# Kernel optimization log

Measured on AMD Instinct MI355X. Metric: run time of the kernel, lower is better.

## Reference

```python
import jax, jax.numpy as jnp
import numpy as np

N_NODES = 20000
N_EDGES = 320000
C = 64  # classes
NEG_SLOPE = 0.2  # DGL GATConv default


def setup_inputs() -> dict:
    key = jax.random.key(0)
    ks = jax.random.split(key, 32)
    dims = [C, 2 * C, 4 * C, 8 * C, 16 * C]
    inp = {}
    inp["feat"] = jax.random.normal(ks[0], (N_NODES, C), jnp.float32)
    k = 1
    for i in range(4):
        din, dout = dims[i], dims[i + 1]
        scale = 1.0 / np.sqrt(din)
        inp[f"W{i+1}"] = jax.random.normal(ks[k], (din, dout), jnp.float32) * scale; k += 1
        inp[f"al{i+1}"] = jax.random.normal(ks[k], (dout,), jnp.float32) * 0.1; k += 1
        inp[f"ar{i+1}"] = jax.random.normal(ks[k], (dout,), jnp.float32) * 0.1; k += 1
        inp[f"b{i+1}"] = jnp.zeros((dout,), jnp.float32)
    inp["relW"] = jax.random.normal(ks[k], (16 * C, C), jnp.float32) * (1.0 / np.sqrt(16 * C)); k += 1
    inp["relB"] = jnp.zeros((C,), jnp.float32)
    inp["src"] = jax.random.randint(ks[k], (N_EDGES,), 0, N_NODES, jnp.int32); k += 1
    inp["dst"] = jax.random.randint(ks[k], (N_EDGES,), 0, N_NODES, jnp.int32); k += 1
    inp["rel"] = jnp.ones((C,), jnp.int32)
    inp["order"] = 1023
    return inp


def _gat_layer(x, W, al, ar, b, src, dst, n_nodes):
    """DGL GATConv (num_heads=1, allow_zero_in_degree=True, activation=tanh)."""
    h = x @ W                                   # [N, D] projected features
    el = h @ al                                 # [N] attn_l score per node
    er = h @ ar                                 # [N] attn_r score per node
    e = jax.nn.leaky_relu(el[src] + er[dst], NEG_SLOPE)          # [E]
    # segment (edge) softmax over incoming edges of each dst node
    m = jax.ops.segment_max(e, dst, num_segments=n_nodes)        # [N]
    ex = jnp.exp(e - m[dst])                                      # [E]
    s = jax.ops.segment_sum(ex, dst, num_segments=n_nodes)       # [N]
    alpha = ex / s[dst]                                           # [E]
    # gather neighbor messages, weight by attention, scatter-add to dst
    out = jax.ops.segment_sum(h[src] * alpha[:, None], dst, num_segments=n_nodes)  # [N, D]
    return jnp.tanh(out + b)


def reference(feat, W1, al1, ar1, b1, W2, al2, ar2, b2, W3, al3, ar3, b3,
              W4, al4, ar4, b4, relW, relB, src, dst, rel, order):
    n = feat.shape[0]
    h = _gat_layer(feat, W1, al1, ar1, b1, src, dst, n)
    h = _gat_layer(h, W2, al2, ar2, b2, src, dst, n)
    h = _gat_layer(h, W3, al3, ar3, b3, src, dst, n)
    h = _gat_layer(h, W4, al4, ar4, b4, src, dst, n)
    embeddings = h[: order + 1]                  # first order+1 node embeddings
    pooling = jnp.mean(embeddings, axis=0)       # [16C]
    logits = pooling @ relW + relB               # [C]
    nz = jnp.nonzero(rel, size=rel.shape[0])[0]  # static-size nonzero (rel is all-ones)
    return logits[nz]
```

## Files before the change

kernel.cpp:

```cpp
#include <hip/hip_runtime.h>
#include <hip/hip_bf16.h>

#define NN 20000
#define NE 320000
#define MPAD 20096
#define ORD 1024
#define NB 79

typedef __hip_bfloat16 bf16;
typedef __attribute__((ext_vector_type(8))) short bf16x8;
typedef __attribute__((ext_vector_type(4))) float f32x4;

#define SCOPE_AGENT __HIP_MEMORY_SCOPE_AGENT

static __device__ __forceinline__ float b2f(bf16 x) { return __bfloat162float(x); }
static __device__ __forceinline__ float bfbits2f(short s) {
    unsigned int u = ((unsigned int)(unsigned short)s) << 16;
    float f; __builtin_memcpy(&f, &u, 4); return f;
}
static __device__ __forceinline__ short f2bfbits(float v) {
    bf16 h = __float2bfloat16(v);
    short s; __builtin_memcpy(&s, &h, 2); return s;
}
static __device__ __forceinline__ unsigned short f2bfu(float v) {
    bf16 h = __float2bfloat16(v);
    unsigned short s; __builtin_memcpy(&s, &h, 2); return s;
}
static __device__ __forceinline__ int aload(const int* p) {
    return __hip_atomic_load(p, __ATOMIC_RELAXED, SCOPE_AGENT);
}
static __device__ __forceinline__ void astore(int* p, int v) {
    __hip_atomic_store(p, v, __ATOMIC_RELAXED, SCOPE_AGENT);
}
static __device__ __forceinline__ void aadd(int* p, int v) {
    __hip_atomic_fetch_add(p, v, __ATOMIC_RELAXED, SCOPE_AGENT);
}
static __device__ __forceinline__ float aloadf(const float* p) {
    return __hip_atomic_load(p, __ATOMIC_RELAXED, SCOPE_AGENT);
}

__global__ void setup_all(const float* __restrict__ feat,
                          const float* __restrict__ W1, const float* __restrict__ al1, const float* __restrict__ ar1,
                          const float* __restrict__ W2, const float* __restrict__ al2, const float* __restrict__ ar2,
                          const float* __restrict__ W3, const float* __restrict__ al3, const float* __restrict__ ar3,
                          const float* __restrict__ W4, const float* __restrict__ al4, const float* __restrict__ ar4,
                          bf16* __restrict__ featb, bf16* __restrict__ wt1,
                          bf16* __restrict__ wt2, bf16* __restrict__ wt3,
                          bf16* __restrict__ wt4, int* __restrict__ counts,
                          int* __restrict__ hglob, int* __restrict__ syncbuf,
                          float* __restrict__ walbuf, float* __restrict__ warbuf) {
    int b = blockIdx.x;
    if (b < 960) {
        const float *W, *al, *ar; int dout, k; float *wal, *war;
        if (b < 64)       { W = W1; al = al1; ar = ar1; dout = 128;  k = b;       wal = walbuf;        war = warbuf; }
        else if (b < 192) { W = W2; al = al2; ar = ar2; dout = 256;  k = b - 64;  wal = walbuf + 512;  war = warbuf + 512; }
        else if (b < 448) { W = W3; al = al3; ar = ar3; dout = 512;  k = b - 192; wal = walbuf + 1024; war = warbuf + 1024; }
        else              { W = W4; al = al4; ar = ar4; dout = 1024; k = b - 448; wal = walbuf + 1536; war = warbuf + 1536; }
        const float* row = W + (long)k * dout;
        float sl = 0.f, sr = 0.f;
        for (int j = threadIdx.x; j < dout; j += 256) {
            float w = row[j];
            sl += w * al[j];
            sr += w * ar[j];
        }
        __shared__ float sbl[256], sbr[256];
        sbl[threadIdx.x] = sl; sbr[threadIdx.x] = sr;
        __syncthreads();
        for (int st = 128; st > 0; st >>= 1) {
            if (threadIdx.x < st) {
                sbl[threadIdx.x] += sbl[threadIdx.x + st];
                sbr[threadIdx.x] += sbr[threadIdx.x + st];
            }
            __syncthreads();
        }
        if (threadIdx.x == 0) { wal[k] = sbl[0]; war[k] = sbr[0]; }
        return;
    }
    int i = (b - 960) * 256 + threadIdx.x;
    if (i < NN) counts[i] = 0;
    if (i < 256) { hglob[i] = 0; syncbuf[i] = 0; }
    if (i < 1280000) { featb[i] = __float2bfloat16(feat[i]); return; }
    i -= 1280000;
    if (i < 8192)  { int r = i >> 7,  c = i & 127;  wt1[c * 64 + r]  = __float2bfloat16(W1[i]); return; }
    i -= 8192;
    if (i < 32768) { int r = i >> 8,  c = i & 255;  wt2[c * 128 + r] = __float2bfloat16(W2[i]); return; }
    i -= 32768;
    if (i < 131072){ int r = i >> 9,  c = i & 511;  wt3[c * 256 + r] = __float2bfloat16(W3[i]); return; }
    i -= 131072;
    if (i < 524288){ int r = i >> 10, c = i & 1023; wt4[c * 512 + r] = __float2bfloat16(W4[i]); return; }
}

__global__ void csr_build(const int* __restrict__ dst, int* __restrict__ counts,
                          int* __restrict__ blocksums, int* __restrict__ blockbase,
                          int* __restrict__ hglob,
                          int* __restrict__ offsets, int* __restrict__ cursor,
                          int* __restrict__ curg, int* __restrict__ sync) {
    int b = blockIdx.x, tid = threadIdx.x;
    if (b < 1250) {
        int i = b * 256 + tid;
        atomicAdd(&counts[dst[i]], 1);
        __syncthreads();
        if (tid == 0) aadd(&sync[(b & 7) * 16], 1);
        return;
    }
    if (b == 1250 + NB) {
        if (tid == 0) while (aload(&sync[128]) != NB) __builtin_amdgcn_s_sleep(2);
        __syncthreads();
        __shared__ int hs[256], bs[256];
        int orig = aload(&hglob[tid]);
        hs[tid] = orig;
        __syncthreads();
        for (int st = 1; st < 256; st <<= 1) {
            int u = (tid >= st) ? hs[tid - st] : 0;
            __syncthreads();
            hs[tid] += u;
            __syncthreads();
        }
        curg[tid] = hs[tid] - orig;
        int v = (tid < NB) ? aload(&blocksums[tid]) : 0;
        bs[tid] = v;
        __syncthreads();
        for (int st = 1; st < 256; st <<= 1) {
            int u = (tid >= st) ? bs[tid - st] : 0;
            __syncthreads();
            bs[tid] += u;
            __syncthreads();
        }
        if (tid < NB) astore(&blockbase[tid], bs[tid] - v);
        __syncthreads();
        if (tid == 0) astore(&sync[132], 1);
        return;
    }
    int pb = b - 1250;
    if (tid == 0) {
        for (;;) {
            int t = 0;
            #pragma unroll
            for (int k = 0; k < 8; k++) t += aload(&sync[k * 16]);
            if (t == 1250) break;
            __builtin_amdgcn_s_sleep(2);
        }
    }
    __syncthreads();
    __shared__ int sc[256], hh[256];
    hh[tid] = 0;
    int i = pb * 256 + tid;
    int c = (i < NN) ? aload(&counts[i]) : 0;
    sc[tid] = c;
    __syncthreads();
    for (int st = 1; st < 256; st <<= 1) {
        int u = (tid >= st) ? sc[tid - st] : 0;
        __syncthreads();
        sc[tid] += u;
        __syncthreads();
    }
    if (tid == 255) astore(&blocksums[pb], sc[255]);
    if (i < NN) { int d = c > 255 ? 255 : c; atomicAdd(&hh[d], 1); }
    __syncthreads();
    if (hh[tid] > 0) atomicAdd(&hglob[tid], hh[tid]);
    __syncthreads();
    if (tid == 0) {
        aadd(&sync[128], 1);
        while (aload(&sync[132]) == 0) __builtin_amdgcn_s_sleep(2);
    }
    __syncthreads();
    int base = aload(&blockbase[pb]);
    int excl = base + sc[tid] - c;
    if (i < NN) { offsets[i] = excl; cursor[i] = excl; }
    if (i == NN - 1) offsets[NN] = excl + c;
}

__global__ void scatter_elr(const int* __restrict__ src, const int* __restrict__ dst,
                            int* __restrict__ cursor, int* __restrict__ esrc,
                            const int* __restrict__ counts, int* __restrict__ curg,
                            int* __restrict__ nodeperm,
                            const bf16* __restrict__ X, const float* __restrict__ wal,
                            const float* __restrict__ war, float* __restrict__ el,
                            float* __restrict__ er) {
    int b = blockIdx.x;
    if (b < 1250) {
        int i = b * 256 + threadIdx.x;
        int p = atomicAdd(&cursor[dst[i]], 1);
        esrc[p] = src[i];
        return;
    }
    if (b < 1250 + NB) {
        __shared__ int hh[256];
        __shared__ int basep[256];
        int tid = threadIdx.x;
        hh[tid] = 0;
        __syncthreads();
        int i = (b - 1250) * 256 + tid;
        int d = 0, rank = 0;
        bool valid = (i < NN);
        if (valid) {
            d = counts[i]; if (d > 255) d = 255;
            rank = atomicAdd(&hh[d], 1);
        }
        __syncthreads();
        if (hh[tid] > 0) basep[tid] = atomicAdd(&curg[tid], hh[tid]);
        __syncthreads();
        if (valid) nodeperm[basep[d] + rank] = i;
        return;
    }
    int idx = (b - 1250 - NB) * 256 + threadIdx.x;
    int node = idx >> 6;
    int lane = threadIdx.x & 63;
    if (node >= NN) return;
    float x = bfbits2f(*((const short*)X + (long)node * 64 + lane));
    float sl = x * wal[lane];
    float sr = x * war[lane];
    #pragma unroll
    for (int o = 32; o > 0; o >>= 1) {
        sl += __shfl_down(sl, o);
        sr += __shfl_down(sr, o);
    }
    if (lane == 0) { el[node] = sl; er[node] = sr; }
}

__global__ void aggregate_sm(const bf16* __restrict__ X,
                             const float* __restrict__ el, const float* __restrict__ er,
                             const int* __restrict__ esrc, const int* __restrict__ off,
                             const int* __restrict__ perm, float* __restrict__ zbuf, int zn,
                             bf16* __restrict__ Y, int din, int log2chunks, int nmax) {
    __shared__ __attribute__((aligned(16))) float alds[32][68];
    {
        int z = blockIdx.x * 256 + threadIdx.x;
        if (z < zn) zbuf[z] = 0.f;
    }
    int chunk = blockIdx.x & ((1 << log2chunks) - 1);
    int nb = blockIdx.x >> log2chunks;
    int sub = threadIdx.x >> 3, sl = threadIdx.x & 7;
    int slot = nb * 32 + sub;
    if (slot >= nmax) return;
    int node = perm ? perm[slot] : slot;
    int s = off[node], e = off[node + 1];
    int deg = e - s;
    bool fast = (deg <= 64);

    float erd = (deg > 0) ? er[node] : 0.f;
    float vmax = -1e30f, inv = 0.f;
    if (fast) {
        float v[8];
        #pragma unroll
        for (int t = 0; t < 8; t++) {
            v[t] = -1e30f;
            int idx = sl + 8 * t;
            if (idx < deg) {
                float x = el[esrc[s + idx]] + erd;
                v[t] = x >= 0.f ? x : 0.2f * x;
            }
            vmax = fmaxf(vmax, v[t]);
        }
        #pragma unroll
        for (int o = 1; o < 8; o <<= 1) vmax = fmaxf(vmax, __shfl_xor(vmax, o));
        float ssum = 0.f;
        #pragma unroll
        for (int t = 0; t < 8; t++) {
            int idx = sl + 8 * t;
            if (idx < deg) { v[t] = __expf(v[t] - vmax); ssum += v[t]; }
        }
        #pragma unroll
        for (int o = 1; o < 8; o <<= 1) ssum += __shfl_xor(ssum, o);
        inv = 1.f / ssum;
        #pragma unroll
        for (int t = 0; t < 8; t++) {
            int idx = sl + 8 * t;
            if (idx < deg) alds[sub][idx] = v[t] * inv;
        }
    } else {
        for (int j = s + sl; j < e; j += 8) {
            float x = el[esrc[j]] + erd;
            x = x >= 0.f ? x : 0.2f * x;
            vmax = fmaxf(vmax, x);
        }
        #pragma unroll
        for (int o = 1; o < 8; o <<= 1) vmax = fmaxf(vmax, __shfl_xor(vmax, o));
        float ssum = 0.f;
        for (int j = s + sl; j < e; j += 8) {
            float x = el[esrc[j]] + erd;
            x = x >= 0.f ? x : 0.2f * x;
            ssum += __expf(x - vmax);
        }
        #pragma unroll
        for (int o = 1; o < 8; o <<= 1) ssum += __shfl_xor(ssum, o);
        inv = 1.f / ssum;
    }

    const short* xb = (const short*)X + chunk * 64 + sl * 8;
    float acc[8] = {0.f,0.f,0.f,0.f,0.f,0.f,0.f,0.f};
    int j = s;
    if (fast) {
        for (; j + 8 <= e; j += 8) {
            int ofs = j - s;
            f32x4 a0 = *(const f32x4*)&alds[sub][ofs];
            f32x4 a1 = *(const f32x4*)&alds[sub][ofs + 4];
            int r[8]; bf16x8 w[8];
            #pragma unroll
            for (int q = 0; q < 8; q++) r[q] = esrc[j + q];
            #pragma unroll
            for (int q = 0; q < 8; q++) w[q] = *(const bf16x8*)(xb + (long)r[q] * din);
            #pragma unroll
            for (int q = 0; q < 4; q++)
                #pragma unroll
                for (int v = 0; v < 8; v++) acc[v] += a0[q] * bfbits2f(w[q][v]);
            #pragma unroll
            for (int q = 0; q < 4; q++)
                #pragma unroll
                for (int v = 0; v < 8; v++) acc[v] += a1[q] * bfbits2f(w[4 + q][v]);
        }
        for (; j + 4 <= e; j += 4) {
            int ofs = j - s;
            f32x4 a0 = *(const f32x4*)&alds[sub][ofs];
            int r[4]; bf16x8 w[4];
            #pragma unroll
            for (int q = 0; q < 4; q++) r[q] = esrc[j + q];
            #pragma unroll
            for (int q = 0; q < 4; q++) w[q] = *(const bf16x8*)(xb + (long)r[q] * din);
            #pragma unroll
            for (int q = 0; q < 4; q++)
                #pragma unroll
                for (int v = 0; v < 8; v++) acc[v] += a0[q] * bfbits2f(w[q][v]);
        }
        for (; j < e; j++) {
            float a = alds[sub][j - s];
            bf16x8 w = *(const bf16x8*)(xb + (long)esrc[j] * din);
            #pragma unroll
            for (int v = 0; v < 8; v++) acc[v] += a * bfbits2f(w[v]);
        }
    } else {
        for (; j + 8 <= e; j += 8) {
            int r[8]; float a[8]; bf16x8 w[8];
            #pragma unroll
            for (int q = 0; q < 8; q++) r[q] = esrc[j + q];
            #pragma unroll
            for (int q = 0; q < 8; q++) {
                float x = el[r[q]] + erd;
                x = x >= 0.f ? x : 0.2f * x;
                a[q] = __expf(x - vmax) * inv;
            }
            #pragma unroll
            for (int q = 0; q < 8; q++) w[q] = *(const bf16x8*)(xb + (long)r[q] * din);
            #pragma unroll
            for (int q = 0; q < 8; q++)
                #pragma unroll
                for (int v = 0; v < 8; v++) acc[v] += a[q] * bfbits2f(w[q][v]);
        }
        for (; j < e; j++) {
            int r = esrc[j];
            float x = el[r] + erd;
            x = x >= 0.f ? x : 0.2f * x;
            float a = __expf(x - vmax) * inv;
            bf16x8 w = *(const bf16x8*)(xb + (long)r * din);
            #pragma unroll
            for (int v = 0; v < 8; v++) acc[v] += a * bfbits2f(w[v]);
        }
    }
    short outv[8];
    #pragma unroll
    for (int v = 0; v < 8; v++) outv[v] = f2bfbits(acc[v]);
    bf16x8 store;
    __builtin_memcpy(&store, outv, sizeof(store));
    *(bf16x8*)((short*)Y + (long)node * din + chunk * 64 + sl * 8) = store;
}

__global__ __launch_bounds__(256, 4)
void gemm_k64(const bf16* __restrict__ A, const bf16* __restrict__ WT,
              const float* __restrict__ bias, bf16* __restrict__ C,
              const float* __restrict__ wal, const float* __restrict__ war,
              float* __restrict__ elp, float* __restrict__ erp) {
    int gw = blockIdx.x * 4 + (threadIdx.x >> 6);
    if (gw >= 2500) return;
    int r0 = (gw >> 1) << 4;
    int col0 = (gw & 1) << 6;
    int lane = threadIdx.x & 63;
    int m = lane & 15, quad = lane >> 4;

    const short* Ab = (const short*)A + (long)(r0 + m) * 64 + quad * 8;
    bf16x8 a0 = *(const bf16x8*)(Ab);
    bf16x8 a1 = *(const bf16x8*)(Ab + 32);

    f32x4 acc[4];
    bf16x8 b0[4], b1[4];
    #pragma unroll
    for (int t = 0; t < 4; t++) {
        acc[t] = (f32x4){0.f, 0.f, 0.f, 0.f};
        const short* Bb = (const short*)WT + (long)(col0 + t * 16 + m) * 64 + quad * 8;
        b0[t] = *(const bf16x8*)(Bb);
        b1[t] = *(const bf16x8*)(Bb + 32);
    }
    #pragma unroll
    for (int t = 0; t < 4; t++) {
        acc[t] = __builtin_amdgcn_mfma_f32_16x16x32_bf16(a0, b0[t], acc[t], 0, 0, 0);
        acc[t] = __builtin_amdgcn_mfma_f32_16x16x32_bf16(a1, b1[t], acc[t], 0, 0, 0);
    }

    float sl4[4] = {0.f, 0.f, 0.f, 0.f};
    float sr4[4] = {0.f, 0.f, 0.f, 0.f};
    #pragma unroll
    for (int t = 0; t < 4; t++) {
        int col = col0 + t * 16 + m;
        float bb = bias[col];
        float wl = wal[col], wrr = war[col];
        #pragma unroll
        for (int r = 0; r < 4; r++) {
            float v = tanhf(acc[t][r] + bb);
            sl4[r] += v * wl;
            sr4[r] += v * wrr;
            float vn = __shfl_xor(v, 1);
            if ((m & 1) == 0) {
                unsigned int pk = (unsigned int)f2bfu(v) | ((unsigned int)f2bfu(vn) << 16);
                int row = r0 + quad * 4 + r;
                *(unsigned int*)((short*)C + (long)row * 128 + col) = pk;
            }
        }
    }
    #pragma unroll
    for (int r = 0; r < 4; r++) {
        float s1 = sl4[r], s2 = sr4[r];
        #pragma unroll
        for (int o = 1; o < 16; o <<= 1) {
            s1 += __shfl_xor(s1, o);
            s2 += __shfl_xor(s2, o);
        }
        if (m == 0) {
            int row = r0 + quad * 4 + r;
            atomicAdd(&elp[row], s1);
            atomicAdd(&erp[row], s2);
        }
    }
}

__global__ __launch_bounds__(256, 4)
void gemm_tiled(const bf16* __restrict__ A, const bf16* __restrict__ WT,
                const float* __restrict__ bias, bf16* __restrict__ C,
                const float* __restrict__ wal, const float* __restrict__ war,
                float* __restrict__ elp, float* __restrict__ erp,
                float* __restrict__ poolacc,
                const float* __restrict__ relW, const float* __restrict__ relB,
                const int* __restrict__ order, const int* __restrict__ rel,
                float* __restrict__ headout,
                int M, int K, int N, int ncols, int nrows) {
    __shared__ short smem[16384];
    short* As = smem;
    short* Bs = smem + 8192;
    int g = blockIdx.x;
    int rowTile = ((g >> 3) / ncols) * 8 + (g & 7);
    int colTile = (g >> 3) % ncols;
    if (rowTile >= nrows) return;
    int row0 = rowTile << 7, col0 = colTile << 7;
    int tid = threadIdx.x;
    int lane = tid & 63, wave = tid >> 6;
    int wr = (wave >> 1) << 6;
    int wc = (wave & 1) << 6;
    int m = lane & 15, quad = lane >> 4;

    f32x4 acc[4][4];
    #pragma unroll
    for (int i = 0; i < 4; i++)
        #pragma unroll
        for (int j = 0; j < 4; j++) acc[i][j] = (f32x4){0.f, 0.f, 0.f, 0.f};

    const short* Ab = (const short*)A;
    const short* Bb = (const short*)WT;
    long ga[4], gb[4];
    #pragma unroll
    for (int n = 0; n < 4; n++) {
        int chunk = n * 256 + tid;
        int row = chunk >> 3;
        int qg = (chunk & 7) ^ (row & 7);
        ga[n] = (long)(row0 + row) * K + qg * 8;
        gb[n] = (long)(col0 + row) * K + qg * 8;
    }

    typedef const __attribute__((address_space(1))) void cgvoid;
    typedef __attribute__((address_space(3))) void lvoid;

    for (int k0 = 0; k0 < K; k0 += 64) {
        __syncthreads();
        #pragma unroll
        for (int n = 0; n < 4; n++)
            __builtin_amdgcn_global_load_lds((cgvoid*)(Ab + ga[n] + k0),
                                             (lvoid*)(As + (n * 256 + tid) * 8), 16, 0, 0);
        #pragma unroll
        for (int n = 0; n < 4; n++)
            __builtin_amdgcn_global_load_lds((cgvoid*)(Bb + gb[n] + k0),
                                             (lvoid*)(Bs + (n * 256 + tid) * 8), 16, 0, 0);
        __syncthreads();
        #pragma unroll
        for (int h = 0; h < 2; h++) {
            bf16x8 af[4], bfr[4];
            #pragma unroll
            for (int s = 0; s < 4; s++) {
                int ra = wr + s * 16 + m;
                int sa = (h * 4 + quad) ^ (ra & 7);
                af[s] = *(const bf16x8*)(As + ra * 64 + sa * 8);
                int rb = wc + s * 16 + m;
                int sb = (h * 4 + quad) ^ (rb & 7);
                bfr[s] = *(const bf16x8*)(Bs + rb * 64 + sb * 8);
            }
            #pragma unroll
            for (int i = 0; i < 4; i++)
                #pragma unroll
                for (int j = 0; j < 4; j++)
                    acc[i][j] = __builtin_amdgcn_mfma_f32_16x16x32_bf16(af[i], bfr[j], acc[i][j], 0, 0, 0);
        }
    }

    float bb[4], walr[4], warr[4];
    #pragma unroll
    for (int j = 0; j < 4; j++) {
        int col = col0 + wc + j * 16 + m;
        bb[j] = bias[col];
        if (elp) { walr[j] = wal[col]; warr[j] = war[col]; }
    }
    float colsum[4] = {0.f, 0.f, 0.f, 0.f};
    __syncthreads();
    short* myep = smem + wave * 1152;
    #pragma unroll
    for (int i = 0; i < 4; i++) {
        float sl4[4] = {0.f, 0.f, 0.f, 0.f};
        float sr4[4] = {0.f, 0.f, 0.f, 0.f};
        #pragma unroll
        for (int j = 0; j < 4; j++) {
            #pragma unroll
            for (int r = 0; r < 4; r++) {
                float v = tanhf(acc[i][j][r] + bb[j]);
                if (elp) { sl4[r] += v * walr[j]; sr4[r] += v * warr[j]; }
                if (poolacc) colsum[j] += v;
                float vn = __shfl_xor(v, 1);
                if ((m & 1) == 0) {
                    unsigned int pk = (unsigned int)f2bfu(v) | ((unsigned int)f2bfu(vn) << 16);
                    *(unsigned int*)(myep + (quad * 4 + r) * 72 + j * 16 + m) = pk;
                }
            }
        }
        #pragma unroll
        for (int pass = 0; pass < 2; pass++) {
            int lr = pass * 8 + (lane >> 3);
            int lc = (lane & 7) * 8;
            bf16x8 v = *(const bf16x8*)(myep + lr * 72 + lc);
            int row = row0 + wr + i * 16 + lr;
            if (row < M)
                *(bf16x8*)((short*)C + (long)row * N + col0 + wc + lc) = v;
        }
        if (elp) {
            #pragma unroll
            for (int r = 0; r < 4; r++) {
                float s1 = sl4[r], s2 = sr4[r];
                #pragma unroll
                for (int o = 1; o < 16; o <<= 1) {
                    s1 += __shfl_xor(s1, o);
                    s2 += __shfl_xor(s2, o);
                }
                if (m == 0) {
                    int row = row0 + wr + i * 16 + quad * 4 + r;
                    if (row < M) {
                        atomicAdd(&elp[row], s1);
                        atomicAdd(&erp[row], s2);
                    }
                }
            }
        }
    }
    if (poolacc) {
        #pragma unroll
        for (int j = 0; j < 4; j++) {
            float cs = colsum[j];
            cs += __shfl_xor(cs, 16);
            cs += __shfl_xor(cs, 32);
            if (quad == 0)
                atomicAdd(&poolacc[col0 + wc + j * 16 + m], cs);
        }
    }
    if (headout) {
        __syncthreads();
        __shared__ int lastf;
        if (tid == 0) {
            unsigned int old = __hip_atomic_fetch_add((unsigned int*)&poolacc[1024], 1u,
                                                      __ATOMIC_RELAXED, SCOPE_AGENT);
            lastf = (old == 63u) ? 1 : 0;
        }
        __syncthreads();
        if (!lastf) return;
        float* ps = (float*)smem;
        float (*part)[64] = (float(*)[64])(smem + 2048);
        for (int i = tid; i < 1024; i += 256) ps[i] = aloadf(&poolacc[i]);
        __syncthreads();
        int t = tid & 63, p = tid >> 6;
        const float* wp = relW + (long)p * 256 * 64 + t;
        float s = 0.f;
        #pragma unroll 8
        for (int c = 0; c < 256; c++) s += ps[p * 256 + c] * wp[(long)c * 64];
        part[p][t] = s;
        __syncthreads();
        if (tid < 64) {
            float rows = (float)(order[0] + 1);
            float lv = (part[0][tid] + part[1][tid] + part[2][tid] + part[3][tid]) / rows + relB[tid];
            int rv = rel[tid];
            unsigned long long mask = __ballot(rv != 0);
            int pos = __popcll(mask & ((1ULL << tid) - 1));
            int count = __popcll(mask);
            float l0 = __shfl(lv, 0);
            if (rv) headout[pos] = lv;
            if (tid >= count) headout[tid] = l0;
        }
    }
}

extern "C" void kernel_launch(void* const* d_in, const int* in_sizes, int n_in,
                              void* d_out, int out_size, void* d_ws, size_t ws_size,
                              hipStream_t stream) {
    const float* feat = (const float*)d_in[0];
    const float* W[4]  = {(const float*)d_in[1], (const float*)d_in[5], (const float*)d_in[9],  (const float*)d_in[13]};
    const float* al[4] = {(const float*)d_in[2], (const float*)d_in[6], (const float*)d_in[10], (const float*)d_in[14]};
    const float* ar[4] = {(const float*)d_in[3], (const float*)d_in[7], (const float*)d_in[11], (const float*)d_in[15]};
    const float* bias[4] = {(const float*)d_in[4], (const float*)d_in[8], (const float*)d_in[12], (const float*)d_in[16]};
    const float* relW = (const float*)d_in[17];
    const float* relB = (const float*)d_in[18];
    const int* src = (const int*)d_in[19];
    const int* dst = (const int*)d_in[20];
    const int* rel = (const int*)d_in[21];
    const int* order = (const int*)d_in[22];

    const int dims[5] = {64, 128, 256, 512, 1024};

    char* p = (char*)d_ws;
    auto carve = [&](size_t bytes) {
        void* r = (void*)p;
        p += (bytes + 255) & ~(size_t)255;
        return r;
    };
    bf16* xbuf = (bf16*)carve((size_t)MPAD * 1024 * sizeof(bf16));
    bf16* ybuf = (bf16*)carve((size_t)MPAD * 512 * sizeof(bf16));
    bf16* featb = (bf16*)carve((size_t)MPAD * 64 * sizeof(bf16));
    bf16* wt[4];
    for (int l = 0; l < 4; l++)
        wt[l] = (bf16*)carve((size_t)dims[l] * dims[l + 1] * sizeof(bf16));
    float* walbuf = (float*)carve(4 * 512 * sizeof(float));
    float* warbuf = (float*)carve(4 * 512 * sizeof(float));
    float* elbuf[2];
    elbuf[0] = (float*)carve((size_t)2 * NN * sizeof(float));
    elbuf[1] = (float*)carve((size_t)2 * NN * sizeof(float));
    int* counts  = (int*)carve((size_t)NN * sizeof(int));
    int* offsets = (int*)carve((size_t)(NN + 1) * sizeof(int));
    int* cursor  = (int*)carve((size_t)NN * sizeof(int));
    int* esrc    = (int*)carve((size_t)NE * sizeof(int));
    int* nodeperm = (int*)carve((size_t)NN * sizeof(int));
    int* blocksums = (int*)carve(128 * sizeof(int));
    int* blockbase = (int*)carve(128 * sizeof(int));
    int* hglob   = (int*)carve(256 * sizeof(int));
    int* curg    = (int*)carve(256 * sizeof(int));
    int* syncbuf = (int*)carve(256 * sizeof(int));
    float* poolsum = (float*)carve(1056 * sizeof(float));

    setup_all<<<960 + 7720, 256, 0, stream>>>(
        feat, W[0], al[0], ar[0], W[1], al[1], ar[1],
        W[2], al[2], ar[2], W[3], al[3], ar[3],
        featb, wt[0], wt[1], wt[2], wt[3], counts, hglob, syncbuf, walbuf, warbuf);

    csr_build<<<1250 + NB + 1, 256, 0, stream>>>(dst, counts, blocksums, blockbase,
                                                 hglob, offsets, cursor, curg, syncbuf);

    scatter_elr<<<1250 + NB + 5000, 256, 0, stream>>>(src, dst, cursor, esrc,
                                                      counts, curg, nodeperm,
                                                      featb, walbuf, warbuf,
                                                      elbuf[0], elbuf[0] + NN);

    const bf16* x = featb;
    const int nrows = MPAD / 128;
    const int nrowsPad = 160;
    const int log2c[4] = {0, 1, 2, 3};
    for (int l = 0; l < 4; l++) {
        int K = dims[l], N = dims[l + 1];
        float* elr_rd = elbuf[l & 1];
        float* elr_wr = elbuf[(l + 1) & 1];
        int nmax  = (l < 3) ? NN : ORD;
        int nodeBlocks = (nmax + 31) / 32;
        const int* aggPerm = (l < 3) ? nodeperm : nullptr;
        float* zbuf = (l < 3) ? elr_wr : poolsum;
        int zn = (l < 3) ? 2 * NN : 1025;
        aggregate_sm<<<nodeBlocks << log2c[l], 256, 0, stream>>>(
            x, elr_rd, elr_rd + NN, esrc, offsets, aggPerm, zbuf, zn, ybuf, K, log2c[l], nmax);
        int ncols = N >> 7;
        if (l == 0) {
            gemm_k64<<<625, 256, 0, stream>>>(ybuf, wt[0], bias[0], xbuf,
                                              walbuf + 512, warbuf + 512,
                                              elr_wr, elr_wr + NN);
        } else if (l < 3) {
            gemm_tiled<<<nrowsPad * ncols, 256, 0, stream>>>(
                ybuf, wt[l], bias[l], xbuf,
                walbuf + (l + 1) * 512, warbuf + (l + 1) * 512,
                elr_wr, elr_wr + NN, nullptr,
                nullptr, nullptr, nullptr, nullptr, nullptr,
                NN, K, N, ncols, nrows);
        } else {
            gemm_tiled<<<8 * ncols, 256, 0, stream>>>(
                ybuf, wt[l], bias[l], xbuf,
                nullptr, nullptr, nullptr, nullptr, poolsum,
                relW, relB, order, rel, (float*)d_out,
                ORD, K, N, ncols, 8);
        }
        x = xbuf;
    }
}
```

Before: 295.9 us.

## Fuse aggregation and GEMM per 128-row tile for first three GAT layers

Adds a fused_layer kernel that performs edge-softmax aggregation for a 128-node tile straight into LDS, then runs the MFMA GEMM with tanh, bias and el/er projection from that tile, for layers 1-3. This drops the intermediate aggregated-feature buffer round trip through global memory and one launch per layer, and writes el/er directly instead of with atomics. The degree-sorted node permutation and its histogram machinery are removed. In exchange only 157 blocks run (about 80 KB LDS each, two per CU), so the gather phase gets far less parallelism than the earlier per-chunk aggregate launches and load balance across high-degree nodes may suffer.

```diff
diff --git a/kernel.cpp b/kernel.cpp
--- a/kernel.cpp
+++ b/kernel.cpp
@@ -47,7 +47,7 @@
                           bf16* __restrict__ featb, bf16* __restrict__ wt1,
                           bf16* __restrict__ wt2, bf16* __restrict__ wt3,
                           bf16* __restrict__ wt4, int* __restrict__ counts,
-                          int* __restrict__ hglob, int* __restrict__ syncbuf,
+                          int* __restrict__ syncbuf,
                           float* __restrict__ walbuf, float* __restrict__ warbuf) {
     int b = blockIdx.x;
     if (b < 960) {
@@ -78,7 +78,7 @@
     }
     int i = (b - 960) * 256 + threadIdx.x;
     if (i < NN) counts[i] = 0;
-    if (i < 256) { hglob[i] = 0; syncbuf[i] = 0; }
+    if (i < 256) syncbuf[i] = 0;
     if (i < 1280000) { featb[i] = __float2bfloat16(feat[i]); return; }
     i -= 1280000;
     if (i < 8192)  { int r = i >> 7,  c = i & 127;  wt1[c * 64 + r]  = __float2bfloat16(W1[i]); return; }
@@ -92,9 +92,8 @@
 
 __global__ void csr_build(const int* __restrict__ dst, int* __restrict__ counts,
                           int* __restrict__ blocksums, int* __restrict__ blockbase,
-                          int* __restrict__ hglob,
                           int* __restrict__ offsets, int* __restrict__ cursor,
-                          int* __restrict__ curg, int* __restrict__ sync) {
+                          int* __restrict__ sync) {
     int b = blockIdx.x, tid = threadIdx.x;
     if (b < 1250) {
         int i = b * 256 + tid;
@@ -106,17 +105,7 @@
     if (b == 1250 + NB) {
         if (tid == 0) while (aload(&sync[128]) != NB) __builtin_amdgcn_s_sleep(2);
         __syncthreads();
-        __shared__ int hs[256], bs[256];
-        int orig = aload(&hglob[tid]);
-        hs[tid] = orig;
-        __syncthreads();
-        for (int st = 1; st < 256; st <<= 1) {
-            int u = (tid >= st) ? hs[tid - st] : 0;
-            __syncthreads();
-            hs[tid] += u;
-            __syncthreads();
-        }
-        curg[tid] = hs[tid] - orig;
+        __shared__ int bs[256];
         int v = (tid < NB) ? aload(&blocksums[tid]) : 0;
         bs[tid] = v;
         __syncthreads();
@@ -142,8 +131,7 @@
         }
     }
     __syncthreads();
-    __shared__ int sc[256], hh[256];
-    hh[tid] = 0;
+    __shared__ int sc[256];
     int i = pb * 256 + tid;
     int c = (i < NN) ? aload(&counts[i]) : 0;
     sc[tid] = c;
@@ -155,9 +143,6 @@
         __syncthreads();
     }
     if (tid == 255) astore(&blocksums[pb], sc[255]);
-    if (i < NN) { int d = c > 255 ? 255 : c; atomicAdd(&hh[d], 1); }
-    __syncthreads();
-    if (hh[tid] > 0) atomicAdd(&hglob[tid], hh[tid]);
     __syncthreads();
     if (tid == 0) {
         aadd(&sync[128], 1);
@@ -172,8 +157,6 @@
 
 __global__ void scatter_elr(const int* __restrict__ src, const int* __restrict__ dst,
                             int* __restrict__ cursor, int* __restrict__ esrc,
-                            const int* __restrict__ counts, int* __restrict__ curg,
-                            int* __restrict__ nodeperm,
                             const bf16* __restrict__ X, const float* __restrict__ wal,
                             const float* __restrict__ war, float* __restrict__ el,
                             float* __restrict__ er) {
@@ -184,26 +167,7 @@
         esrc[p] = src[i];
         return;
     }
-    if (b < 1250 + NB) {
-        __shared__ int hh[256];
-        __shared__ int basep[256];
-        int tid = threadIdx.x;
-        hh[tid] = 0;
-        __syncthreads();
-        int i = (b - 1250) * 256 + tid;
-        int d = 0, rank = 0;
-        bool valid = (i < NN);
-        if (valid) {
-            d = counts[i]; if (d > 255) d = 255;
-            rank = atomicAdd(&hh[d], 1);
-        }
-        __syncthreads();
-        if (hh[tid] > 0) basep[tid] = atomicAdd(&curg[tid], hh[tid]);
-        __syncthreads();
-        if (valid) nodeperm[basep[d] + rank] = i;
-        return;
-    }
-    int idx = (b - 1250 - NB) * 256 + threadIdx.x;
+    int idx = (b - 1250) * 256 + threadIdx.x;
     int node = idx >> 6;
     int lane = threadIdx.x & 63;
     if (node >= NN) return;
@@ -218,10 +182,283 @@
     if (lane == 0) { el[node] = sl; er[node] = sr; }
 }
 
+__global__ __launch_bounds__(256, 2)
+void fused_layer(const bf16* __restrict__ X,
+                 const float* __restrict__ el, const float* __restrict__ er,
+                 const int* __restrict__ esrc, const int* __restrict__ off,
+                 const bf16* __restrict__ WT, const float* __restrict__ bias,
+                 bf16* __restrict__ C,
+                 const float* __restrict__ wal, const float* __restrict__ war,
+                 float* __restrict__ elo, float* __restrict__ ero,
+                 int K, int ncols) {
+    __shared__ __attribute__((aligned(16))) short smem[40960];
+    short* As = smem;
+    short* Bs = smem + 32768;
+    float (*alds)[68] = (float(*)[68])Bs;
+
+    int row0 = blockIdx.x << 7;
+    int tid = threadIdx.x, lane = tid & 63, wave = tid >> 6;
+    int sub = tid >> 3, sl = tid & 7;
+    int nch = K >> 6;
+
+    for (int nb = 0; nb < 4; nb++) {
+        int nl = nb * 32 + sub;
+        int node = row0 + nl;
+        bool valid = node < NN;
+        int s = 0, deg = 0;
+        float erd = 0.f, vmax = -1e30f, inv = 0.f;
+        bool fast = true;
+        if (valid) {
+            s = off[node];
+            deg = off[node + 1] - s;
+            fast = (deg <= 64);
+            erd = (deg > 0) ? er[node] : 0.f;
+        }
+        int e = s + deg;
+        if (valid) {
+            if (fast) {
+                float v[8];
+                #pragma unroll
+                for (int t = 0; t < 8; t++) {
+                    v[t] = -1e30f;
+                    int idx = sl + 8 * t;
+                    if (idx < deg) {
+                        float x = el[esrc[s + idx]] + erd;
+                        v[t] = x >= 0.f ? x : 0.2f * x;
+                    }
+                    vmax = fmaxf(vmax, v[t]);
+                }
+                #pragma unroll
+                for (int o = 1; o < 8; o <<= 1) vmax = fmaxf(vmax, __shfl_xor(vmax, o));
+                float ssum = 0.f;
+                #pragma unroll
+                for (int t = 0; t < 8; t++) {
+                    int idx = sl + 8 * t;
+                    if (idx < deg) { v[t] = __expf(v[t] - vmax); ssum += v[t]; }
+                }
+                #pragma unroll
+                for (int o = 1; o < 8; o <<= 1) ssum += __shfl_xor(ssum, o);
+                inv = 1.f / ssum;
+                #pragma unroll
+                for (int t = 0; t < 8; t++) {
+                    int idx = sl + 8 * t;
+                    if (idx < deg) alds[sub][idx] = v[t] * inv;
+                }
+            } else {
+                for (int j = s + sl; j < e; j += 8) {
+                    float x = el[esrc[j]] + erd;
+                    x = x >= 0.f ? x : 0.2f * x;
+                    vmax = fmaxf(vmax, x);
+                }
+                #pragma unroll
+                for (int o = 1; o < 8; o <<= 1) vmax = fmaxf(vmax, __shfl_xor(vmax, o));
+                float ssum = 0.f;
+                for (int j = s + sl; j < e; j += 8) {
+                    float x = el[esrc[j]] + erd;
+                    x = x >= 0.f ? x : 0.2f * x;
+                    ssum += __expf(x - vmax);
+                }
+                #pragma unroll
+                for (int o = 1; o < 8; o <<= 1) ssum += __shfl_xor(ssum, o);
+                inv = 1.f / ssum;
+            }
+        }
+        for (int c = 0; c < nch; c++) {
+            float acc[8] = {0.f,0.f,0.f,0.f,0.f,0.f,0.f,0.f};
+            if (valid && deg > 0) {
+                const short* xb = (const short*)X + c * 64 + sl * 8;
+                int j = s;
+                if (fast) {
+                    for (; j + 8 <= e; j += 8) {
+                        int ofs = j - s;
+                        f32x4 a0 = *(const f32x4*)&alds[sub][ofs];
+                        f32x4 a1 = *(const f32x4*)&alds[sub][ofs + 4];
+                        int r[8]; bf16x8 w[8];
+                        #pragma unroll
+                        for (int q = 0; q < 8; q++) r[q] = esrc[j + q];
+                        #pragma unroll
+                        for (int q = 0; q < 8; q++) w[q] = *(const bf16x8*)(xb + (long)r[q] * K);
+                        #pragma unroll
+                        for (int q = 0; q < 4; q++)
+                            #pragma unroll
+                            for (int v = 0; v < 8; v++) acc[v] += a0[q] * bfbits2f(w[q][v]);
+                        #pragma unroll
+                        for (int q = 0; q < 4; q++)
+                            #pragma unroll
+                            for (int v = 0; v < 8; v++) acc[v] += a1[q] * bfbits2f(w[4 + q][v]);
+                    }
+                    for (; j + 4 <= e; j += 4) {
+                        int ofs = j - s;
+                        f32x4 a0 = *(const f32x4*)&alds[sub][ofs];
+                        int r[4]; bf16x8 w[4];
+                        #pragma unroll
+                        for (int q = 0; q < 4; q++) r[q] = esrc[j + q];
+                        #pragma unroll
+                        for (int q = 0; q < 4; q++) w[q] = *(const bf16x8*)(xb + (long)r[q] * K);
+                        #pragma unroll
+                        for (int q = 0; q < 4; q++)
+                            #pragma unroll
+                            for (int v = 0; v < 8; v++) acc[v] += a0[q] * bfbits2f(w[q][v]);
+                    }
+                    for (; j < e; j++) {
+                        float a = alds[sub][j - s];
+                        bf16x8 w = *(const bf16x8*)(xb + (long)esrc[j] * K);
+                        #pragma unroll
+                        for (int v = 0; v < 8; v++) acc[v] += a * bfbits2f(w[v]);
+                    }
+                } else {
+                    for (; j < e; j++) {
+                        int r = esrc[j];
+                        float x = el[r] + erd;
+                        x = x >= 0.f ? x : 0.2f * x;
+                        float a = __expf(x - vmax) * inv;
+                        bf16x8 w = *(const bf16x8*)(xb + (long)r * K);
+                        #pragma unroll
+                        for (int v = 0; v < 8; v++) acc[v] += a * bfbits2f(w[v]);
+                    }
+                }
+            }
+            short outv[8];
+            #pragma unroll
+            for (int v = 0; v < 8; v++) outv[v] = f2bfbits(acc[v]);
+            bf16x8 st;
+            __builtin_memcpy(&st, outv, sizeof(st));
+            int qs = (c * 8 + sl) ^ (nl & 7);
+            *(bf16x8*)(As + nl * K + qs * 8) = st;
+        }
+    }
+    __syncthreads();
+
+    int m = lane & 15, quad = lane >> 4;
+    int wr = (wave >> 1) << 6;
+    int wc = (wave & 1) << 6;
+    float slacc[4][4], sracc[4][4];
+    #pragma unroll
+    for (int i = 0; i < 4; i++)
+        #pragma unroll
+        for (int r = 0; r < 4; r++) { slacc[i][r] = 0.f; sracc[i][r] = 0.f; }
+
+    typedef const __attribute__((address_space(1))) void cgvoid;
+    typedef __attribute__((address_space(3))) void lvoid;
+    int N = ncols << 7;
+
+    for (int ct = 0; ct < ncols; ct++) {
+        int col0 = ct << 7;
+        f32x4 acc[4][4];
+        #pragma unroll
+        for (int i = 0; i < 4; i++)
+            #pragma unroll
+            for (int j = 0; j < 4; j++) acc[i][j] = (f32x4){0.f, 0.f, 0.f, 0.f};
+
+        for (int k0 = 0; k0 < K; k0 += 64) {
+            __syncthreads();
+            #pragma unroll
+            for (int n = 0; n < 4; n++) {
+                int chunk = n * 256 + tid;
+                int brow = chunk >> 3;
+                int qg = (chunk & 7) ^ (brow & 7);
+                __builtin_amdgcn_global_load_lds(
+                    (cgvoid*)((const short*)WT + (long)(col0 + brow) * K + k0 + qg * 8),
+                    (lvoid*)(Bs + (n * 256 + tid) * 8), 16, 0, 0);
+            }
+            __syncthreads();
+            int kq = k0 >> 3;
+            #pragma unroll
+            for (int h = 0; h < 2; h++) {
+                bf16x8 af[4], bfr[4];
+                #pragma unroll
+                for (int ss = 0; ss < 4; ss++) {
+                    int ra = wr + ss * 16 + m;
+                    int sa = (kq + h * 4 + quad) ^ (ra & 7);
+                    af[ss] = *(const bf16x8*)(As + ra * K + sa * 8);
+                    int rb = wc + ss * 16 + m;
+                    int sb = (h * 4 + quad) ^ (rb & 7);
+                    bfr[ss] = *(const bf16x8*)(Bs + rb * 64 + sb * 8);
+                }
+                #pragma unroll
+                for (int i = 0; i < 4; i++)
+                    #pragma unroll
+                    for (int j = 0; j < 4; j++)
+                        acc[i][j] = __builtin_amdgcn_mfma_f32_16x16x32_bf16(af[i], bfr[j], acc[i][j], 0, 0, 0);
+            }
+        }
+        __syncthreads();
+
+        float bb[4], walr[4], warr[4];
+        #pragma unroll
+        for (int j = 0; j < 4; j++) {
+            int col = col0 + wc + j * 16 + m;
+            bb[j] = bias[col];
+            walr[j] = wal[col]; warr[j] = war[col];
+        }
+        short* myep = Bs + wave * 1152;
+        #pragma unroll
+        for (int i = 0; i < 4; i++) {
+            #pragma unroll
+            for (int j = 0; j < 4; j++) {
+                #pragma unroll
+                for (int r = 0; r < 4; r++) {
+                    float v = tanhf(acc[i][j][r] + bb[j]);
+                    slacc[i][r] += v * walr[j];
+                    sracc[i][r] += v * warr[j];
+                    float vn = __shfl_xor(v, 1);
+                    if ((m & 1) == 0) {
+                        unsigned int pk = (unsigned int)f2bfu(v) | ((unsigned int)f2bfu(vn) << 16);
+                        *(unsigned int*)(myep + (quad * 4 + r) * 72 + j * 16 + m) = pk;
+                    }
+                }
+            }
+            #pragma unroll
+            for (int pass = 0; pass < 2; pass++) {
+                int lr = pass * 8 + (lane >> 3);
+                int lc = (lane & 7) * 8;
+                bf16x8 v = *(const bf16x8*)(myep + lr * 72 + lc);
+                int row = row0 + wr + i * 16 + lr;
+                if (row < NN)
+                    *(bf16x8*)((short*)C + (long)row * N + col0 + wc + lc) = v;
+            }
+        }
+    }
+
+    __syncthreads();
+    float* scr = (float*)smem;
+    #pragma unroll
+    for (int i = 0; i < 4; i++) {
+        #pragma unroll
+        for (int r = 0; r < 4; r++) {
+            float s1 = slacc[i][r], s2 = sracc[i][r];
+            #pragma unroll
+            for (int o = 1; o < 16; o <<= 1) {
+                s1 += __shfl_xor(s1, o);
+                s2 += __shfl_xor(s2, o);
+            }
+            slacc[i][r] = s1; sracc[i][r] = s2;
+            if ((wave & 1) == 1 && m == 0) {
+                int lr = wr + i * 16 + quad * 4 + r;
+                scr[lr * 2] = s1; scr[lr * 2 + 1] = s2;
+            }
+        }
+    }
+    __syncthreads();
+    if ((wave & 1) == 0 && m == 0) {
+        #pragma unroll
+        for (int i = 0; i < 4; i++)
+            #pragma unroll
+            for (int r = 0; r < 4; r++) {
+                int lr = wr + i * 16 + quad * 4 + r;
+                int row = row0 + lr;
+                if (row < NN) {
+                    elo[row] = slacc[i][r] + scr[lr * 2];
+                    ero[row] = sracc[i][r] + scr[lr * 2 + 1];
+                }
+            }
+    }
+}
+
 __global__ void aggregate_sm(const bf16* __restrict__ X,
                              const float* __restrict__ el, const float* __restrict__ er,
                              const int* __restrict__ esrc, const int* __restrict__ off,
-                             const int* __restrict__ perm, float* __restrict__ zbuf, int zn,
+                             float* __restrict__ zbuf, int zn,
                              bf16* __restrict__ Y, int din, int log2chunks, int nmax) {
     __shared__ __attribute__((aligned(16))) float alds[32][68];
     {
@@ -233,7 +470,7 @@
     int sub = threadIdx.x >> 3, sl = threadIdx.x & 7;
     int slot = nb * 32 + sub;
     if (slot >= nmax) return;
-    int node = perm ? perm[slot] : slot;
+    int node = slot;
     int s = off[node], e = off[node + 1];
     int deg = e - s;
     bool fast = (deg <= 64);
@@ -329,23 +566,6 @@
             for (int v = 0; v < 8; v++) acc[v] += a * bfbits2f(w[v]);
         }
     } else {
-        for (; j + 8 <= e; j += 8) {
-            int r[8]; float a[8]; bf16x8 w[8];
-            #pragma unroll
-            for (int q = 0; q < 8; q++) r[q] = esrc[j + q];
-            #pragma unroll
-            for (int q = 0; q < 8; q++) {
-                float x = el[r[q]] + erd;
-                x = x >= 0.f ? x : 0.2f * x;
-                a[q] = __expf(x - vmax) * inv;
-            }
-            #pragma unroll
-            for (int q = 0; q < 8; q++) w[q] = *(const bf16x8*)(xb + (long)r[q] * din);
-            #pragma unroll
-            for (int q = 0; q < 8; q++)
-                #pragma unroll
-                for (int v = 0; v < 8; v++) acc[v] += a[q] * bfbits2f(w[q][v]);
-        }
         for (; j < e; j++) {
             int r = esrc[j];
             float x = el[r] + erd;
@@ -365,77 +585,8 @@
 }
 
 __global__ __launch_bounds__(256, 4)
-void gemm_k64(const bf16* __restrict__ A, const bf16* __restrict__ WT,
-              const float* __restrict__ bias, bf16* __restrict__ C,
-              const float* __restrict__ wal, const float* __restrict__ war,
-              float* __restrict__ elp, float* __restrict__ erp) {
-    int gw = blockIdx.x * 4 + (threadIdx.x >> 6);
-    if (gw >= 2500) return;
-    int r0 = (gw >> 1) << 4;
-    int col0 = (gw & 1) << 6;
-    int lane = threadIdx.x & 63;
-    int m = lane & 15, quad = lane >> 4;
-
-    const short* Ab = (const short*)A + (long)(r0 + m) * 64 + quad * 8;
-    bf16x8 a0 = *(const bf16x8*)(Ab);
-    bf16x8 a1 = *(const bf16x8*)(Ab + 32);
-
-    f32x4 acc[4];
-    bf16x8 b0[4], b1[4];
-    #pragma unroll
-    for (int t = 0; t < 4; t++) {
-        acc[t] = (f32x4){0.f, 0.f, 0.f, 0.f};
-        const short* Bb = (const short*)WT + (long)(col0 + t * 16 + m) * 64 + quad * 8;
-        b0[t] = *(const bf16x8*)(Bb);
-        b1[t] = *(const bf16x8*)(Bb + 32);
-    }
-    #pragma unroll
-    for (int t = 0; t < 4; t++) {
-        acc[t] = __builtin_amdgcn_mfma_f32_16x16x32_bf16(a0, b0[t], acc[t], 0, 0, 0);
-        acc[t] = __builtin_amdgcn_mfma_f32_16x16x32_bf16(a1, b1[t], acc[t], 0, 0, 0);
-    }
-
-    float sl4[4] = {0.f, 0.f, 0.f, 0.f};
-    float sr4[4] = {0.f, 0.f, 0.f, 0.f};
-    #pragma unroll
-    for (int t = 0; t < 4; t++) {
-        int col = col0 + t * 16 + m;
-        float bb = bias[col];
-        float wl = wal[col], wrr = war[col];
-        #pragma unroll
-        for (int r = 0; r < 4; r++) {
-            float v = tanhf(acc[t][r] + bb);
-            sl4[r] += v * wl;
-            sr4[r] += v * wrr;
-            float vn = __shfl_xor(v, 1);
-            if ((m & 1) == 0) {
-                unsigned int pk = (unsigned int)f2bfu(v) | ((unsigned int)f2bfu(vn) << 16);
-                int row = r0 + quad * 4 + r;
-                *(unsigned int*)((short*)C + (long)row * 128 + col) = pk;
-            }
-        }
-    }
-    #pragma unroll
-    for (int r = 0; r < 4; r++) {
-        float s1 = sl4[r], s2 = sr4[r];
-        #pragma unroll
-        for (int o = 1; o < 16; o <<= 1) {
-            s1 += __shfl_xor(s1, o);
-            s2 += __shfl_xor(s2, o);
-        }
-        if (m == 0) {
-            int row = r0 + quad * 4 + r;
-            atomicAdd(&elp[row], s1);
-            atomicAdd(&erp[row], s2);
-        }
-    }
-}
-
-__global__ __launch_bounds__(256, 4)
 void gemm_tiled(const bf16* __restrict__ A, const bf16* __restrict__ WT,
                 const float* __restrict__ bias, bf16* __restrict__ C,
-                const float* __restrict__ wal, const float* __restrict__ war,
-                float* __restrict__ elp, float* __restrict__ erp,
                 float* __restrict__ poolacc,
                 const float* __restrict__ relW, const float* __restrict__ relB,
                 const int* __restrict__ order, const int* __restrict__ rel,
@@ -507,27 +658,20 @@
         }
     }
 
-    float bb[4], walr[4], warr[4];
+    float bb[4];
     #pragma unroll
-    for (int j = 0; j < 4; j++) {
-        int col = col0 + wc + j * 16 + m;
-        bb[j] = bias[col];
-        if (elp) { walr[j] = wal[col]; warr[j] = war[col]; }
-    }
+    for (int j = 0; j < 4; j++) bb[j] = bias[col0 + wc + j * 16 + m];
     float colsum[4] = {0.f, 0.f, 0.f, 0.f};
     __syncthreads();
     short* myep = smem + wave * 1152;
     #pragma unroll
     for (int i = 0; i < 4; i++) {
-        float sl4[4] = {0.f, 0.f, 0.f, 0.f};
-        float sr4[4] = {0.f, 0.f, 0.f, 0.f};
         #pragma unroll
         for (int j = 0; j < 4; j++) {
             #pragma unroll
             for (int r = 0; r < 4; r++) {
                 float v = tanhf(acc[i][j][r] + bb[j]);
-                if (elp) { sl4[r] += v * walr[j]; sr4[r] += v * warr[j]; }
-                if (poolacc) colsum[j] += v;
+                colsum[j] += v;
                 float vn = __shfl_xor(v, 1);
                 if ((m & 1) == 0) {
                     unsigned int pk = (unsigned int)f2bfu(v) | ((unsigned int)f2bfu(vn) << 16);
@@ -544,67 +688,45 @@
             if (row < M)
                 *(bf16x8*)((short*)C + (long)row * N + col0 + wc + lc) = v;
         }
-        if (elp) {
-            #pragma unroll
-            for (int r = 0; r < 4; r++) {
-                float s1 = sl4[r], s2 = sr4[r];
-                #pragma unroll
-                for (int o = 1; o < 16; o <<= 1) {
-                    s1 += __shfl_xor(s1, o);
-                    s2 += __shfl_xor(s2, o);
-                }
-                if (m == 0) {
-                    int row = row0 + wr + i * 16 + quad * 4 + r;
-                    if (row < M) {
-                        atomicAdd(&elp[row], s1);
-                        atomicAdd(&erp[row], s2);
-                    }
-                }
-            }
-        }
-    }
-    if (poolacc) {
-        #pragma unroll
-        for (int j = 0; j < 4; j++) {
-            float cs = colsum[j];
-            cs += __shfl_xor(cs, 16);
-            cs += __shfl_xor(cs, 32);
-            if (quad == 0)
-                atomicAdd(&poolacc[col0 + wc + j * 16 + m], cs);
-        }
-    }
-    if (headout) {
-        __syncthreads();
-        __shared__ int lastf;
-        if (tid == 0) {
-            unsigned int old = __hip_atomic_fetch_add((unsigned int*)&poolacc[1024], 1u,
-                                                      __ATOMIC_RELAXED, SCOPE_AGENT);
-            lastf = (old == 63u) ? 1 : 0;
-        }
-        __syncthreads();
-        if (!lastf) return;
-        float* ps = (float*)smem;
-        float (*part)[64] = (float(*)[64])(smem + 2048);
-        for (int i = tid; i < 1024; i += 256) ps[i] = aloadf(&poolacc[i]);
-        __syncthreads();
-        int t = tid & 63, p = tid >> 6;
-        const float* wp = relW + (long)p * 256 * 64 + t;
-        float s = 0.f;
-        #pragma unroll 8
-        for (int c = 0; c < 256; c++) s += ps[p * 256 + c] * wp[(long)c * 64];
-        part[p][t] = s;
-        __syncthreads();
-        if (tid < 64) {
-            float rows = (float)(order[0] + 1);
-            float lv = (part[0][tid] + part[1][tid] + part[2][tid] + part[3][tid]) / rows + relB[tid];
-            int rv = rel[tid];
-            unsigned long long mask = __ballot(rv != 0);
-            int pos = __popcll(mask & ((1ULL << tid) - 1));
-            int count = __popcll(mask);
-            float l0 = __shfl(lv, 0);
-            if (rv) headout[pos] = lv;
-            if (tid >= count) headout[tid] = l0;
-        }
+    }
+    #pragma unroll
+    for (int j = 0; j < 4; j++) {
+        float cs = colsum[j];
+        cs += __shfl_xor(cs, 16);
+        cs += __shfl_xor(cs, 32);
+        if (quad == 0)
+            atomicAdd(&poolacc[col0 + wc + j * 16 + m], cs);
+    }
+    __syncthreads();
+    __shared__ int lastf;
+    if (tid == 0) {
+        unsigned int old = __hip_atomic_fetch_add((unsigned int*)&poolacc[1024], 1u,
+                                                  __ATOMIC_RELAXED, SCOPE_AGENT);
+        lastf = (old == 63u) ? 1 : 0;
+    }
+    __syncthreads();
+    if (!lastf) return;
+    float* ps = (float*)smem;
+    float (*part)[64] = (float(*)[64])(smem + 2048);
+    for (int i = tid; i < 1024; i += 256) ps[i] = aloadf(&poolacc[i]);
+    __syncthreads();
+    int t = tid & 63, p = tid >> 6;
+    const float* wp = relW + (long)p * 256 * 64 + t;
+    float s = 0.f;
+    #pragma unroll 8
+    for (int c = 0; c < 256; c++) s += ps[p * 256 + c] * wp[(long)c * 64];
+    part[p][t] = s;
+    __syncthreads();
+    if (tid < 64) {
+        float rows = (float)(order[0] + 1);
+        float lv = (part[0][tid] + part[1][tid] + part[2][tid] + part[3][tid]) / rows + relB[tid];
+        int rv = rel[tid];
+        unsigned long long mask = __ballot(rv != 0);
+        int pos = __popcll(mask & ((1ULL << tid) - 1));
+        int count = __popcll(mask);
+        float l0 = __shfl(lv, 0);
+        if (rv) headout[pos] = lv;
+        if (tid >= count) headout[tid] = l0;
     }
 }
 
@@ -631,8 +753,9 @@
         p += (bytes + 255) & ~(size_t)255;
         return r;
     };
-    bf16* xbuf = (bf16*)carve((size_t)MPAD * 1024 * sizeof(bf16));
-    bf16* ybuf = (bf16*)carve((size_t)MPAD * 512 * sizeof(bf16));
+    bf16* xA = (bf16*)carve((size_t)MPAD * 512 * sizeof(bf16));
+    bf16* xB = (bf16*)carve((size_t)MPAD * 256 * sizeof(bf16));
+    bf16* y4 = (bf16*)carve((size_t)ORD * 512 * sizeof(bf16));
     bf16* featb = (bf16*)carve((size_t)MPAD * 64 * sizeof(bf16));
     bf16* wt[4];
     for (int l = 0; l < 4; l++)
@@ -646,61 +769,40 @@
     int* offsets = (int*)carve((size_t)(NN + 1) * sizeof(int));
     int* cursor  = (int*)carve((size_t)NN * sizeof(int));
     int* esrc    = (int*)carve((size_t)NE * sizeof(int));
-    int* nodeperm = (int*)carve((size_t)NN * sizeof(int));
     int* blocksums = (int*)carve(128 * sizeof(int));
     int* blockbase = (int*)carve(128 * sizeof(int));
-    int* hglob   = (int*)carve(256 * sizeof(int));
-    int* curg    = (int*)carve(256 * sizeof(int));
     int* syncbuf = (int*)carve(256 * sizeof(int));
     float* poolsum = (float*)carve(1056 * sizeof(float));
 
     setup_all<<<960 + 7720, 256, 0, stream>>>(
         feat, W[0], al[0], ar[0], W[1], al[1], ar[1],
         W[2], al[2], ar[2], W[3], al[3], ar[3],
-        featb, wt[0], wt[1], wt[2], wt[3], counts, hglob, syncbuf, walbuf, warbuf);
+        featb, wt[0], wt[1], wt[2], wt[3], counts, syncbuf, walbuf, warbuf);
 
     csr_build<<<1250 + NB + 1, 256, 0, stream>>>(dst, counts, blocksums, blockbase,
-                                                 hglob, offsets, cursor, curg, syncbuf);
-
-    scatter_elr<<<1250 + NB + 5000, 256, 0, stream>>>(src, dst, cursor, esrc,
-                                                      counts, curg, nodeperm,
-                                                      featb, walbuf, warbuf,
-                                                      elbuf[0], elbuf[0] + NN);
-
-    const bf16* x = featb;
-    const int nrows = MPAD / 128;
-    const int nrowsPad = 160;
-    const int log2c[4] = {0, 1, 2, 3};
-    for (int l = 0; l < 4; l++) {
-        int K = dims[l], N = dims[l + 1];
-        float* elr_rd = elbuf[l & 1];
-        float* elr_wr = elbuf[(l + 1) & 1];
-        int nmax  = (l < 3) ? NN : ORD;
-        int nodeBlocks = (nmax + 31) / 32;
-        const int* aggPerm = (l < 3) ? nodeperm : nullptr;
-        float* zbuf = (l < 3) ? elr_wr : poolsum;
-        int zn = (l < 3) ? 2 * NN : 1025;
-        aggregate_sm<<<nodeBlocks << log2c[l], 256, 0, stream>>>(
-            x, elr_rd, elr_rd + NN, esrc, offsets, aggPerm, zbuf, zn, ybuf, K, log2c[l], nmax);
-        int ncols = N >> 7;
-        if (l == 0) {
-            gemm_k64<<<625, 256, 0, stream>>>(ybuf, wt[0], bias[0], xbuf,
-                                              walbuf + 512, warbuf + 512,
-                                              elr_wr, elr_wr + NN);
-        } else if (l < 3) {
-            gemm_tiled<<<nrowsPad * ncols, 256, 0, stream>>>(
-                ybuf, wt[l], bias[l], xbuf,
-                walbuf + (l + 1) * 512, warbuf + (l + 1) * 512,
-                elr_wr, elr_wr + NN, nullptr,
-                nullptr, nullptr, nullptr, nullptr, nullptr,
-                NN, K, N, ncols, nrows);
-        } else {
-            gemm_tiled<<<8 * ncols, 256, 0, stream>>>(
-                ybuf, wt[l], bias[l], xbuf,
-                nullptr, nullptr, nullptr, nullptr, poolsum,
-                relW, relB, order, rel, (float*)d_out,
-                ORD, K, N, ncols, 8);
-        }
-        x = xbuf;
-    }
-}
+                                                 offsets, cursor, syncbuf);
+
+    scatter_elr<<<1250 + 5000, 256, 0, stream>>>(src, dst, cursor, esrc,
+                                                 featb, walbuf, warbuf,
+                                                 elbuf[0], elbuf[0] + NN);
+
+    fused_layer<<<157, 256, 0, stream>>>(featb, elbuf[0], elbuf[0] + NN, esrc, offsets,
+                                         wt[0], bias[0], xA,
+                                         walbuf + 512, warbuf + 512,
+                                         elbuf[1], elbuf[1] + NN, 64, 1);
+    fused_layer<<<157, 256, 0, stream>>>(xA, elbuf[1], elbuf[1] + NN, esrc, offsets,
+                                         wt[1], bias[1], xB,
+                                         walbuf + 1024, warbuf + 1024,
+                                         elbuf[0], elbuf[0] + NN, 128, 2);
+    fused_layer<<<157, 256, 0, stream>>>(xB, elbuf[0], elbuf[0] + NN, esrc, offsets,
+                                         wt[2], bias[2], xA,
+                                         walbuf + 1536, warbuf + 1536,
+                                         elbuf[1], elbuf[1] + NN, 256, 4);
+
+    aggregate_sm<<<32 << 3, 256, 0, stream>>>(xA, elbuf[1], elbuf[1] + NN, esrc, offsets,
+                                              poolsum, 1025, y4, 512, 3, ORD);
+
+    gemm_tiled<<<8 * 8, 256, 0, stream>>>(y4, wt[3], bias[3], xB, poolsum,
+                                          relW, relB, order, rel, (float*)d_out,
+                                          ORD, 512, 1024, 8, 8);
+}
```

Measured after the change: 440.8 us. 48.9% more time.
